# Optimization experiments

Measured on AMD Instinct MI355X. Metric: run time of the kernel, lower is better.

## Reference

```python
import jax, jax.numpy as jnp
import numpy as np

F = 128
NRBF = 20
CUTOFF = 5.0
L = 3
NZ = 100
F2 = F // 2
N = 10000
E = 256000
NMOL = 100
EPS = 1e-8


def setup_inputs() -> dict:
    key = jax.random.key(0)
    ks = jax.random.split(key, 20)
    xyz = jax.random.uniform(ks[0], (N, 3), jnp.float32) * 10.0
    z = jax.random.randint(ks[1], (N,), 0, NZ)
    nbrs = jax.random.randint(ks[2], (E, 2), 0, N)
    # avoid self-edges (would give zero distance in the sinc RBF)
    nbrs = nbrs.at[:, 1].set(jnp.where(nbrs[:, 1] == nbrs[:, 0], (nbrs[:, 1] + 1) % N, nbrs[:, 1]))
    mol_idx = jnp.sort(jax.random.randint(ks[3], (N,), 0, NMOL))

    def p(k, shape, scale=0.05):
        return jax.random.normal(k, shape, jnp.float32) * scale

    return dict(
        xyz=xyz, z=z, nbrs=nbrs, mol_idx=mol_idx,
        emb=p(ks[4], (NZ, F), 1.0),
        msg_W1=p(ks[5], (L, F, F)), msg_b1=jnp.zeros((L, F), jnp.float32),
        msg_W2=p(ks[6], (L, F, 3 * F)), msg_b2=jnp.zeros((L, 3 * F), jnp.float32),
        dist_W=p(ks[7], (L, NRBF, 3 * F)), dist_b=jnp.zeros((L, 3 * F), jnp.float32),
        upd_U=p(ks[8], (L, F, F)), upd_V=p(ks[9], (L, F, F)),
        upd_W1=p(ks[10], (L, 2 * F, F)), upd_b1=jnp.zeros((L, F), jnp.float32),
        upd_W2=p(ks[11], (L, F, 3 * F)), upd_b2=jnp.zeros((L, 3 * F), jnp.float32),
        read_W1=p(ks[12], (F, F2)), read_b1=jnp.zeros((F2,), jnp.float32),
        read_W2=p(ks[13], (F2, 1)), read_b2=jnp.zeros((1,), jnp.float32),
    )


def _painn(xyz, emb, msg_W1, msg_b1, msg_W2, msg_b2, dist_W, dist_b,
           upd_U, upd_V, upd_W1, upd_b1, upd_W2, upd_b2,
           read_W1, read_b1, read_W2, read_b2, z, nbrs, mol_idx):
    idx_i = nbrs[:, 0]
    idx_j = nbrs[:, 1]
    r_ij = xyz[idx_j] - xyz[idx_i]                       # [E,3]
    d = jnp.sqrt(jnp.sum(r_ij * r_ij, -1) + EPS)          # [E]
    unit = r_ij / d[:, None]
    # sinc radial basis + cosine cutoff envelope
    nvec = jnp.arange(1, NRBF + 1, dtype=xyz.dtype)
    rbf = jnp.sin(nvec[None, :] * jnp.pi * d[:, None] / CUTOFF) / d[:, None]   # [E,NRBF]
    fcut = 0.5 * (jnp.cos(jnp.pi * d / CUTOFF) + 1.0) * (d < CUTOFF)           # [E]

    s_i = emb[z]                                          # [N,F]
    v_i = jnp.zeros((xyz.shape[0], F, 3), xyz.dtype)      # [N,F,3]

    for l in range(L):
        # message block: invariant filter on nodes, gather to edges
        phi = (jax.nn.silu(s_i @ msg_W1[l] + msg_b1[l]) @ msg_W2[l] + msg_b2[l])[idx_j]  # [E,3F]
        w_s = (rbf @ dist_W[l] + dist_b[l]) * fcut[:, None]                               # [E,3F]
        inv = (phi * w_s).reshape(-1, 3, F)
        ds_edge = inv[:, 0]                                                               # [E,F]
        dv_edge = inv[:, 1][:, :, None] * v_i[idx_j] + inv[:, 2][:, :, None] * unit[:, None, :]  # [E,F,3]
        s_i = s_i + jax.ops.segment_sum(ds_edge, idx_i, num_segments=s_i.shape[0])
        v_i = v_i + jax.ops.segment_sum(dv_edge, idx_i, num_segments=s_i.shape[0])

        # update block: channel-mixing of vectors + gated scalar/vector residuals
        u_v = jnp.einsum('nfv,fg->ngv', v_i, upd_U[l])
        v_v = jnp.einsum('nfv,fg->ngv', v_i, upd_V[l])
        vnorm = jnp.sqrt(jnp.sum(v_v * v_v, -1) + EPS)                                    # [N,F]
        a = (jax.nn.silu(jnp.concatenate([s_i, vnorm], -1) @ upd_W1[l] + upd_b1[l])
             @ upd_W2[l] + upd_b2[l]).reshape(-1, 3, F)
        dv = u_v * a[:, 0][:, :, None]
        ds = a[:, 1] * jnp.sum(u_v * v_v, -1) + a[:, 2]
        s_i = s_i + ds
        v_i = v_i + dv

    atom_e = jax.nn.silu(s_i @ read_W1 + read_b1) @ read_W2 + read_b2                     # [N,1]
    energy = jax.ops.segment_sum(atom_e[:, 0], mol_idx, num_segments=NMOL)                # [NMOL]
    return energy


def reference(xyz, z, nbrs, mol_idx, emb, msg_W1, msg_b1, msg_W2, msg_b2,
              dist_W, dist_b, upd_U, upd_V, upd_W1, upd_b1, upd_W2, upd_b2,
              read_W1, read_b1, read_W2, read_b2):
    return _painn(xyz, emb, msg_W1, msg_b1, msg_W2, msg_b2, dist_W, dist_b,
                  upd_U, upd_V, upd_W1, upd_b1, upd_W2, upd_b2,
                  read_W1, read_b1, read_W2, read_b2, z, nbrs, mol_idx)
```

## Files before the change

kernel.cpp:

```cpp
#include <hip/hip_runtime.h>
#include <hip/hip_bf16.h>
#include <math.h>

#define NA 10000
#define NE 256000
#define FDIM 128
#define F3 384
#define NRBF 20
#define NLAYERS 3
#define NMOLS 100
#define CAP 96
#define WROW 388
#define PACK_BLOCKS 2288
#define CUTOFF_F 5.0f
#define EPS_F 1e-8f
#define PI_F 3.14159265358979323846f

typedef __attribute__((ext_vector_type(8))) short bf16x8;
typedef __attribute__((ext_vector_type(4))) float f32x4;

struct pv6 { unsigned int u0, u1, u2; };

__device__ __forceinline__ float silu_f(float x) { return x / (1.0f + __expf(-x)); }

__device__ __forceinline__ unsigned short f2bf(float x) {
  unsigned u = __float_as_uint(x);
  return (unsigned short)((u + 0x7FFFu + ((u >> 16) & 1u)) >> 16);
}
__device__ __forceinline__ float bf2f(unsigned short u) {
  return __uint_as_float(((unsigned)u) << 16);
}
__device__ __forceinline__ float lo_f(unsigned int u) { return bf2f((unsigned short)(u & 0xFFFFu)); }
__device__ __forceinline__ float hi_f(unsigned int u) { return bf2f((unsigned short)(u >> 16)); }

__device__ __forceinline__ void pack_one(const float* __restrict__ src,
                                         unsigned short* __restrict__ dst,
                                         int loc, int per, int N) {
  int lay = loc / per;
  int kn = loc - lay * per;
  int k = kn / N, n = kn - k * N;
  int kb = k >> 5, q = (k >> 3) & 3, j = k & 7, nt = n >> 4, c = n & 15;
  int NT = N >> 4;
  dst[(size_t)lay * per + (((kb * NT + nt) * 64 + (q * 16 + c)) * 8 + j)] = f2bf(src[loc]);
}

__device__ __forceinline__ void pack_dw(const float* __restrict__ dW,
                                        const float* __restrict__ db,
                                        unsigned short* __restrict__ dst, int loc) {
  int lay = loc / 12288;
  int kn = loc - lay * 12288;
  int k = kn / 384, n = kn - k * 384;
  float val = 0.0f;
  if (k < NRBF) val = dW[lay * NRBF * 384 + k * 384 + n];
  else if (k == NRBF) val = db[lay * 384 + n];
  int q = (k >> 3) & 3, j = k & 7, nt = n >> 4, c = n & 15;
  dst[(size_t)lay * 12288 + ((nt * 64 + (q * 16 + c)) * 8 + j)] = f2bf(val);
}

__global__ __launch_bounds__(256) void prep_kernel(
    const float* __restrict__ msgW1, const float* __restrict__ msgW2,
    const float* __restrict__ updU, const float* __restrict__ updV,
    const float* __restrict__ updW1, const float* __restrict__ updW2,
    const float* __restrict__ rW1, const float* __restrict__ distW,
    const float* __restrict__ distb, unsigned short* __restrict__ dst,
    const float* __restrict__ xyz, const int* __restrict__ nbrs,
    float* __restrict__ unitv, unsigned short* __restrict__ rbf_bf,
    float* __restrict__ fcut,
    int* __restrict__ deg, int* __restrict__ slot_e, int* __restrict__ slot_j) {
  int b = blockIdx.x;
  if (b < PACK_BLOCKS) {
    int t = b * 256 + threadIdx.x;
    if (t < 49152) pack_one(msgW1, dst, t, 16384, 128);
    else if (t < 196608) pack_one(msgW2, dst + 49152, t - 49152, 49152, 384);
    else if (t < 245760) pack_one(updU, dst + 196608, t - 196608, 16384, 128);
    else if (t < 294912) pack_one(updV, dst + 245760, t - 245760, 16384, 128);
    else if (t < 393216) pack_one(updW1, dst + 294912, t - 294912, 32768, 128);
    else if (t < 540672) pack_one(updW2, dst + 393216, t - 393216, 49152, 384);
    else if (t < 548864) pack_one(rW1, dst + 540672, t - 540672, 8192, 64);
    else if (t < 585728) pack_dw(distW, distb, dst + 548864, t - 548864);
    return;
  }
  int e = (b - PACK_BLOCKS) * 256 + threadIdx.x;
  if (e >= NE) return;
  int i = nbrs[2 * e + 0], j = nbrs[2 * e + 1];
  float rx = xyz[3 * j + 0] - xyz[3 * i + 0];
  float ry = xyz[3 * j + 1] - xyz[3 * i + 1];
  float rz = xyz[3 * j + 2] - xyz[3 * i + 2];
  float d = sqrtf(rx * rx + ry * ry + rz * rz + EPS_F);
  if (d >= CUTOFF_F) return;
  float invd = 1.0f / d;
  float fc = 0.5f * (__cosf(PI_F * d / CUTOFF_F) + 1.0f);
  unitv[3 * e + 0] = rx * invd;
  unitv[3 * e + 1] = ry * invd;
  unitv[3 * e + 2] = rz * invd;
  fcut[e] = fc;
  float base = PI_F * d / CUTOFF_F;
  float sc = invd * fc;
#pragma unroll
  for (int k = 0; k < NRBF; k++)
    rbf_bf[(size_t)e * NRBF + k] = f2bf(__sinf((float)(k + 1) * base) * sc);
  int pos = atomicAdd(&deg[i], 1);
  if (pos < CAP) {
    slot_e[i * CAP + pos] = e;
    slot_j[i * CAP + pos] = j;
  }
}

__global__ __launch_bounds__(256) void msg0_mfma_kernel(
    const float* __restrict__ emb, const int* __restrict__ z, float* __restrict__ s_out,
    const unsigned short* __restrict__ pW1, const float* __restrict__ b1,
    const unsigned short* __restrict__ pW2, const float* __restrict__ b2,
    pv6* __restrict__ cmb) {
  __shared__ bf16x8 sA[4 * 64];
  __shared__ bf16x8 hA[4 * 64];
  int a0 = blockIdx.x * 16;
  int t = threadIdx.x;
  int lane = t & 63, w = t >> 6;
  {
    int kb = t >> 6, l = t & 63;
    int m = l & 15, q = l >> 4;
    int zi = z[a0 + m];
    const float* sp = emb + (size_t)zi * FDIM + kb * 32 + q * 8;
    float* so = s_out + (size_t)(a0 + m) * FDIM + kb * 32 + q * 8;
    bf16x8 c;
#pragma unroll
    for (int j = 0; j < 8; j++) {
      float v = sp[j];
      so[j] = v;
      c[j] = (short)f2bf(v);
    }
    sA[kb * 64 + l] = c;
  }
  __syncthreads();
  f32x4 accH[2];
#pragma unroll
  for (int t2 = 0; t2 < 2; t2++)
#pragma unroll
    for (int r = 0; r < 4; r++) accH[t2][r] = 0.0f;
  const bf16x8* W1f = (const bf16x8*)pW1;
#pragma unroll
  for (int kb = 0; kb < 4; kb++) {
    bf16x8 a = sA[kb * 64 + lane];
#pragma unroll
    for (int t2 = 0; t2 < 2; t2++) {
      bf16x8 b = W1f[(kb * 8 + 2 * w + t2) * 64 + lane];
      accH[t2] = __builtin_amdgcn_mfma_f32_16x16x32_bf16(a, b, accH[t2], 0, 0, 0);
    }
  }
  short* hs = (short*)hA;
#pragma unroll
  for (int t2 = 0; t2 < 2; t2++) {
    int n = w * 32 + t2 * 16 + (lane & 15);
    int kb = n >> 5, q = (n >> 3) & 3, j = n & 7;
    float bias = b1[n];
#pragma unroll
    for (int r = 0; r < 4; r++) {
      int m = (lane >> 4) * 4 + r;
      hs[(kb * 64 + q * 16 + m) * 8 + j] = (short)f2bf(silu_f(accH[t2][r] + bias));
    }
  }
  __syncthreads();
  f32x4 accP[3][2];
#pragma unroll
  for (int c3 = 0; c3 < 3; c3++)
#pragma unroll
    for (int t2 = 0; t2 < 2; t2++)
#pragma unroll
      for (int r = 0; r < 4; r++) accP[c3][t2][r] = 0.0f;
  const bf16x8* W2f = (const bf16x8*)pW2;
#pragma unroll
  for (int kb = 0; kb < 4; kb++) {
    bf16x8 a = hA[kb * 64 + lane];
#pragma unroll
    for (int c3 = 0; c3 < 3; c3++)
#pragma unroll
      for (int t2 = 0; t2 < 2; t2++) {
        bf16x8 b = W2f[(kb * 24 + c3 * 8 + 2 * w + t2) * 64 + lane];
        accP[c3][t2] = __builtin_amdgcn_mfma_f32_16x16x32_bf16(a, b, accP[c3][t2], 0, 0, 0);
      }
  }
#pragma unroll
  for (int t2 = 0; t2 < 2; t2++) {
    int g = (2 * w + t2) * 16 + (lane & 15);
    float bb0 = b2[g], bb1 = b2[FDIM + g], bb2 = b2[2 * FDIM + g];
#pragma unroll
    for (int r = 0; r < 4; r++) {
      int m = (lane >> 4) * 4 + r;
      unsigned p0 = f2bf(accP[0][t2][r] + bb0);
      unsigned p1 = f2bf(accP[1][t2][r] + bb1);
      unsigned p2 = f2bf(accP[2][t2][r] + bb2);
      pv6 rec;
      rec.u0 = p0 | (p1 << 16);
      rec.u1 = p2;
      rec.u2 = 0;
      cmb[(size_t)(a0 + m) * FDIM + g] = rec;
    }
  }
}

__global__ __launch_bounds__(128) void edge_kernel(
    const pv6* __restrict__ cmb, unsigned short* __restrict__ v_lin,
    float* __restrict__ s, const unsigned short* __restrict__ pDW,
    const int* __restrict__ deg, const int* __restrict__ slot_e,
    const int* __restrict__ slot_j, const unsigned short* __restrict__ rbf_bf,
    const float* __restrict__ fcut, const float* __restrict__ unitv) {
  __shared__ bf16x8 aLDS[64];
  __shared__ unsigned short w_lds[16][WROW];
  __shared__ float l_u[16][3];
  __shared__ int l_j[16];
  int i = blockIdx.x;
  int t = threadIdx.x;
  int f = t;
  int lane = t & 63, w = t >> 6;
  int cnt = deg[i];
  if (cnt > CAP) cnt = CAP;
  int base = i * CAP;
  float acc_s = 0.f, av0 = 0.f, av1 = 0.f, av2 = 0.f;
  const bf16x8* Bf = (const bf16x8*)pDW;
  for (int c0 = 0; c0 < cnt; c0 += 16) {
    int ccnt = cnt - c0;
    if (ccnt > 16) ccnt = 16;
    __syncthreads();
    if (t < 64) {
      int m = t & 15, q = t >> 4;
      bf16x8 a;
#pragma unroll
      for (int j = 0; j < 8; j++) a[j] = 0;
      int p = c0 + m;
      if (p < cnt) {
        int e = slot_e[base + p];
        const unsigned short* rb = rbf_bf + (size_t)e * NRBF;
#pragma unroll
        for (int j = 0; j < 8; j++) {
          int k = q * 8 + j;
          if (k < NRBF) a[j] = (short)rb[k];
          else if (k == NRBF) a[j] = (short)f2bf(fcut[e]);
        }
      }
      aLDS[t] = a;
    } else if (t < 80) {
      int idx = t - 64;
      int p = c0 + idx;
      if (p < cnt) {
        int e = slot_e[base + p];
        l_j[idx] = slot_j[base + p];
        l_u[idx][0] = unitv[3 * e + 0];
        l_u[idx][1] = unitv[3 * e + 1];
        l_u[idx][2] = unitv[3 * e + 2];
      }
    }
    __syncthreads();
    {
      bf16x8 a = aLDS[lane];
      int n0 = lane & 15, m0 = (lane >> 4) * 4;
#pragma unroll
      for (int tt = 0; tt < 12; tt++) {
        int nt = 12 * w + tt;
        f32x4 acc;
#pragma unroll
        for (int r = 0; r < 4; r++) acc[r] = 0.0f;
        acc = __builtin_amdgcn_mfma_f32_16x16x32_bf16(a, Bf[nt * 64 + lane], acc, 0, 0, 0);
        int n = nt * 16 + n0;
#pragma unroll
        for (int r = 0; r < 4; r++) w_lds[m0 + r][n] = f2bf(acc[r]);
      }
    }
    __syncthreads();
    int pp = 0;
    for (; pp + 4 <= ccnt; pp += 4) {
      pv6 R[4];
#pragma unroll
      for (int u = 0; u < 4; u++) R[u] = cmb[(size_t)l_j[pp + u] * FDIM + f];
#pragma unroll
      for (int u = 0; u < 4; u++) {
        float p0 = lo_f(R[u].u0), p1 = hi_f(R[u].u0), p2 = lo_f(R[u].u1);
        float v0 = hi_f(R[u].u1), v1 = lo_f(R[u].u2), v2 = hi_f(R[u].u2);
        float w0 = bf2f(w_lds[pp + u][f]), w1 = bf2f(w_lds[pp + u][FDIM + f]),
              w2 = bf2f(w_lds[pp + u][2 * FDIM + f]);
        acc_s += p0 * w0;
        float i1 = p1 * w1, i2 = p2 * w2;
        av0 += i1 * v0 + i2 * l_u[pp + u][0];
        av1 += i1 * v1 + i2 * l_u[pp + u][1];
        av2 += i1 * v2 + i2 * l_u[pp + u][2];
      }
    }
    for (; pp < ccnt; pp++) {
      pv6 R0 = cmb[(size_t)l_j[pp] * FDIM + f];
      float p0 = lo_f(R0.u0), p1 = hi_f(R0.u0), p2 = lo_f(R0.u1);
      float v0 = hi_f(R0.u1), v1 = lo_f(R0.u2), v2 = hi_f(R0.u2);
      float w0 = bf2f(w_lds[pp][f]), w1 = bf2f(w_lds[pp][FDIM + f]),
            w2 = bf2f(w_lds[pp][2 * FDIM + f]);
      acc_s += p0 * w0;
      float i1 = p1 * w1, i2 = p2 * w2;
      av0 += i1 * v0 + i2 * l_u[pp][0];
      av1 += i1 * v1 + i2 * l_u[pp][1];
      av2 += i1 * v2 + i2 * l_u[pp][2];
    }
  }
  {
    pv6 RI = cmb[(size_t)i * FDIM + f];
    av0 += hi_f(RI.u1);
    av1 += lo_f(RI.u2);
    av2 += hi_f(RI.u2);
  }
  unsigned short* vlo = v_lin + (size_t)i * F3;
  vlo[f] = f2bf(av0);
  vlo[FDIM + f] = f2bf(av1);
  vlo[2 * FDIM + f] = f2bf(av2);
  s[(size_t)i * FDIM + f] += acc_s;
}

__global__ __launch_bounds__(256) void upd_fused_kernel(
    float* __restrict__ s, const unsigned short* __restrict__ v_lin,
    pv6* __restrict__ cmb,
    const unsigned short* __restrict__ pU, const unsigned short* __restrict__ pV,
    const unsigned short* __restrict__ pW1, const float* __restrict__ b1,
    const unsigned short* __restrict__ pW2, const float* __restrict__ b2,
    int mode,
    const unsigned short* __restrict__ pMW1, const float* __restrict__ mb1,
    const unsigned short* __restrict__ pMW2, const float* __restrict__ mb2,
    const unsigned short* __restrict__ pRW1, const float* __restrict__ rb1,
    const float* __restrict__ rW2, const float* __restrict__ rb2,
    float* __restrict__ atom_e) {
  __shared__ bf16x8 vAf[3 * 4 * 64];
  __shared__ bf16x8 catA[8 * 64];
  __shared__ bf16x8 hA[4 * 64];
  __shared__ float red[4][16];
  int a0 = blockIdx.x * 16;
  int t = threadIdx.x;
  int lane = t & 63, w = t >> 6;
  {
    int l = t & 63, kb = (t >> 6) & 3;
    int m = l & 15, q = l >> 4;
#pragma unroll
    for (int rt = 0; rt < 3; rt++) {
      vAf[(rt * 4 + kb) * 64 + l] =
          *(const bf16x8*)(v_lin + (size_t)(a0 + m) * F3 + rt * FDIM + kb * 32 + q * 8);
    }
    const float* sp = s + (size_t)(a0 + m) * FDIM + kb * 32 + q * 8;
    bf16x8 c;
#pragma unroll
    for (int j = 0; j < 8; j++) c[j] = (short)f2bf(sp[j]);
    catA[kb * 64 + l] = c;
  }
  __syncthreads();
  f32x4 accU[3][2], accV[3][2];
#pragma unroll
  for (int rt = 0; rt < 3; rt++)
#pragma unroll
    for (int t2 = 0; t2 < 2; t2++)
#pragma unroll
      for (int r = 0; r < 4; r++) { accU[rt][t2][r] = 0.0f; accV[rt][t2][r] = 0.0f; }
  const bf16x8* Uf = (const bf16x8*)pU;
  const bf16x8* Vf = (const bf16x8*)pV;
#pragma unroll
  for (int kb = 0; kb < 4; kb++) {
    bf16x8 bu[2], bv[2];
#pragma unroll
    for (int t2 = 0; t2 < 2; t2++) {
      bu[t2] = Uf[(kb * 8 + 2 * w + t2) * 64 + lane];
      bv[t2] = Vf[(kb * 8 + 2 * w + t2) * 64 + lane];
    }
#pragma unroll
    for (int rt = 0; rt < 3; rt++) {
      bf16x8 a = vAf[(rt * 4 + kb) * 64 + lane];
#pragma unroll
      for (int t2 = 0; t2 < 2; t2++) {
        accU[rt][t2] = __builtin_amdgcn_mfma_f32_16x16x32_bf16(a, bu[t2], accU[rt][t2], 0, 0, 0);
        accV[rt][t2] = __builtin_amdgcn_mfma_f32_16x16x32_bf16(a, bv[t2], accV[rt][t2], 0, 0, 0);
      }
    }
  }
  short* cs = (short*)catA;
#pragma unroll
  for (int t2 = 0; t2 < 2; t2++) {
    int g = w * 32 + t2 * 16 + (lane & 15);
    int k = 128 + g;
    int kb = k >> 5, q = (k >> 3) & 3, j = k & 7;
#pragma unroll
    for (int r = 0; r < 4; r++) {
      int m = (lane >> 4) * 4 + r;
      float x0 = accV[0][t2][r], x1 = accV[1][t2][r], x2 = accV[2][t2][r];
      cs[(kb * 64 + q * 16 + m) * 8 + j] = (short)f2bf(sqrtf(x0 * x0 + x1 * x1 + x2 * x2 + EPS_F));
    }
  }
  __syncthreads();
  f32x4 accH[2];
#pragma unroll
  for (int t2 = 0; t2 < 2; t2++)
#pragma unroll
    for (int r = 0; r < 4; r++) accH[t2][r] = 0.0f;
  const bf16x8* W1f = (const bf16x8*)pW1;
#pragma unroll
  for (int kb = 0; kb < 8; kb++) {
    bf16x8 a = catA[kb * 64 + lane];
#pragma unroll
    for (int t2 = 0; t2 < 2; t2++) {
      bf16x8 b = W1f[(kb * 8 + 2 * w + t2) * 64 + lane];
      accH[t2] = __builtin_amdgcn_mfma_f32_16x16x32_bf16(a, b, accH[t2], 0, 0, 0);
    }
  }
  short* hs = (short*)hA;
#pragma unroll
  for (int t2 = 0; t2 < 2; t2++) {
    int n = w * 32 + t2 * 16 + (lane & 15);
    int kb = n >> 5, q = (n >> 3) & 3, j = n & 7;
    float bias = b1[n];
#pragma unroll
    for (int r = 0; r < 4; r++) {
      int m = (lane >> 4) * 4 + r;
      hs[(kb * 64 + q * 16 + m) * 8 + j] = (short)f2bf(silu_f(accH[t2][r] + bias));
    }
  }
  __syncthreads();
  f32x4 accA[3][2];
#pragma unroll
  for (int c3 = 0; c3 < 3; c3++)
#pragma unroll
    for (int t2 = 0; t2 < 2; t2++)
#pragma unroll
      for (int r = 0; r < 4; r++) accA[c3][t2][r] = 0.0f;
  const bf16x8* W2f = (const bf16x8*)pW2;
#pragma unroll
  for (int kb = 0; kb < 4; kb++) {
    bf16x8 a = hA[kb * 64 + lane];
#pragma unroll
    for (int c3 = 0; c3 < 3; c3++)
#pragma unroll
      for (int t2 = 0; t2 < 2; t2++) {
        bf16x8 b = W2f[(kb * 24 + c3 * 8 + 2 * w + t2) * 64 + lane];
        accA[c3][t2] = __builtin_amdgcn_mfma_f32_16x16x32_bf16(a, b, accA[c3][t2], 0, 0, 0);
      }
  }
  const short* vls = (const short*)vAf;
  unsigned short v0keep[2][4];
#pragma unroll
  for (int t2 = 0; t2 < 2; t2++) {
    int g = w * 32 + t2 * 16 + (lane & 15);
    float bb0 = b2[g], bb1 = b2[FDIM + g], bb2 = b2[2 * FDIM + g];
    int kb = g >> 5, q = (g >> 3) & 3, j = g & 7;
#pragma unroll
    for (int r = 0; r < 4; r++) {
      int m = (lane >> 4) * 4 + r;
      int n = a0 + m;
      float a0v = accA[0][t2][r] + bb0;
      float a1v = accA[1][t2][r] + bb1;
      float a2v = accA[2][t2][r] + bb2;
      float dot = accU[0][t2][r] * accV[0][t2][r] + accU[1][t2][r] * accV[1][t2][r] +
                  accU[2][t2][r] * accV[2][t2][r];
      float s_new = s[(size_t)n * FDIM + g] + a1v * dot + a2v;
      if (mode == 0) {
        s[(size_t)n * FDIM + g] = s_new;
        float nv[3];
#pragma unroll
        for (int c = 0; c < 3; c++) {
          float vold = bf2f((unsigned short)vls[(((c * 4 + kb) * 64) + (q * 16 + m)) * 8 + j]);
          nv[c] = vold + a0v * accU[c][t2][r];
        }
        v0keep[t2][r] = f2bf(nv[0]);
        cmb[(size_t)n * FDIM + g].u2 = (unsigned)f2bf(nv[1]) | ((unsigned)f2bf(nv[2]) << 16);
      }
      cs[(kb * 64 + q * 16 + m) * 8 + j] = (short)f2bf(s_new);
    }
  }
  __syncthreads();
  if (mode == 0) {
    f32x4 accH2[2];
#pragma unroll
    for (int t2 = 0; t2 < 2; t2++)
#pragma unroll
      for (int r = 0; r < 4; r++) accH2[t2][r] = 0.0f;
    const bf16x8* MW1f = (const bf16x8*)pMW1;
#pragma unroll
    for (int kb = 0; kb < 4; kb++) {
      bf16x8 a = catA[kb * 64 + lane];
#pragma unroll
      for (int t2 = 0; t2 < 2; t2++) {
        bf16x8 b = MW1f[(kb * 8 + 2 * w + t2) * 64 + lane];
        accH2[t2] = __builtin_amdgcn_mfma_f32_16x16x32_bf16(a, b, accH2[t2], 0, 0, 0);
      }
    }
#pragma unroll
    for (int t2 = 0; t2 < 2; t2++) {
      int n = w * 32 + t2 * 16 + (lane & 15);
      int kb = n >> 5, q = (n >> 3) & 3, j = n & 7;
      float bias = mb1[n];
#pragma unroll
      for (int r = 0; r < 4; r++) {
        int m = (lane >> 4) * 4 + r;
        hs[(kb * 64 + q * 16 + m) * 8 + j] = (short)f2bf(silu_f(accH2[t2][r] + bias));
      }
    }
    __syncthreads();
    f32x4 accP[3][2];
#pragma unroll
    for (int c3 = 0; c3 < 3; c3++)
#pragma unroll
      for (int t2 = 0; t2 < 2; t2++)
#pragma unroll
        for (int r = 0; r < 4; r++) accP[c3][t2][r] = 0.0f;
    const bf16x8* MW2f = (const bf16x8*)pMW2;
#pragma unroll
    for (int kb = 0; kb < 4; kb++) {
      bf16x8 a = hA[kb * 64 + lane];
#pragma unroll
      for (int c3 = 0; c3 < 3; c3++)
#pragma unroll
        for (int t2 = 0; t2 < 2; t2++) {
          bf16x8 b = MW2f[(kb * 24 + c3 * 8 + 2 * w + t2) * 64 + lane];
          accP[c3][t2] = __builtin_amdgcn_mfma_f32_16x16x32_bf16(a, b, accP[c3][t2], 0, 0, 0);
        }
    }
#pragma unroll
    for (int t2 = 0; t2 < 2; t2++) {
      int g = (2 * w + t2) * 16 + (lane & 15);
      float bb0 = mb2[g], bb1 = mb2[FDIM + g], bb2v = mb2[2 * FDIM + g];
#pragma unroll
      for (int r = 0; r < 4; r++) {
        int m = (lane >> 4) * 4 + r;
        unsigned p0 = f2bf(accP[0][t2][r] + bb0);
        unsigned p1 = f2bf(accP[1][t2][r] + bb1);
        unsigned p2 = f2bf(accP[2][t2][r] + bb2v);
        pv6* rec = &cmb[(size_t)(a0 + m) * FDIM + g];
        rec->u0 = p0 | (p1 << 16);
        rec->u1 = p2 | ((unsigned)v0keep[t2][r] << 16);
      }
    }
  } else {
    f32x4 acc;
#pragma unroll
    for (int r = 0; r < 4; r++) acc[r] = 0.0f;
    const bf16x8* RW1f = (const bf16x8*)pRW1;
#pragma unroll
    for (int kb = 0; kb < 4; kb++) {
      bf16x8 a = catA[kb * 64 + lane];
      bf16x8 b = RW1f[(kb * 4 + w) * 64 + lane];
      acc = __builtin_amdgcn_mfma_f32_16x16x32_bf16(a, b, acc, 0, 0, 0);
    }
    int col = w * 16 + (lane & 15);
    float bias = rb1[col], w2v = rW2[col];
    float val[4];
#pragma unroll
    for (int r = 0; r < 4; r++) val[r] = silu_f(acc[r] + bias) * w2v;
#pragma unroll
    for (int off = 1; off < 16; off <<= 1)
#pragma unroll
      for (int r = 0; r < 4; r++) val[r] += __shfl_xor(val[r], off, 64);
    if ((lane & 15) == 0) {
#pragma unroll
      for (int r = 0; r < 4; r++) red[w][(lane >> 4) * 4 + r] = val[r];
    }
    __syncthreads();
    if (t < 16) {
      atom_e[a0 + t] = red[0][t] + red[1][t] + red[2][t] + red[3][t] + rb2[0];
    }
  }
}

__global__ __launch_bounds__(256) void mol_reduce_kernel(
    const float* __restrict__ atom_e, const int* __restrict__ mol_idx,
    float* __restrict__ out) {
  __shared__ float molsum[NMOLS];
  int t = threadIdx.x;
  if (t < NMOLS) molsum[t] = 0.0f;
  __syncthreads();
  int n = blockIdx.x * 256 + t;
  if (n < NA) atomicAdd(&molsum[mol_idx[n]], atom_e[n]);
  __syncthreads();
  if (t < NMOLS && molsum[t] != 0.0f) atomicAdd(&out[t], molsum[t]);
}

extern "C" void kernel_launch(void* const* d_in, const int* in_sizes, int n_in,
                              void* d_out, int out_size, void* d_ws, size_t ws_size,
                              hipStream_t stream) {
  const float* xyz = (const float*)d_in[0];
  const int* z = (const int*)d_in[1];
  const int* nbrs = (const int*)d_in[2];
  const int* mol = (const int*)d_in[3];
  const float* emb = (const float*)d_in[4];
  const float* msgW1 = (const float*)d_in[5];
  const float* msgb1 = (const float*)d_in[6];
  const float* msgW2 = (const float*)d_in[7];
  const float* msgb2 = (const float*)d_in[8];
  const float* distW = (const float*)d_in[9];
  const float* distb = (const float*)d_in[10];
  const float* updU = (const float*)d_in[11];
  const float* updV = (const float*)d_in[12];
  const float* updW1 = (const float*)d_in[13];
  const float* updb1 = (const float*)d_in[14];
  const float* updW2 = (const float*)d_in[15];
  const float* updb2 = (const float*)d_in[16];
  const float* rW1 = (const float*)d_in[17];
  const float* rb1 = (const float*)d_in[18];
  const float* rW2 = (const float*)d_in[19];
  const float* rb2 = (const float*)d_in[20];

  float* ws = (float*)d_ws;
  float* s = ws;      ws += (size_t)NA * FDIM;
  float* fcut = ws;   ws += (size_t)NE;
  float* unitv = ws;  ws += (size_t)NE * 3;
  float* atom_e = ws; ws += (size_t)NA;
  int* deg = (int*)ws;
  int* slot_e = deg + NA;
  int* slot_j = slot_e + NA * CAP;
  unsigned short* pk = (unsigned short*)(((uintptr_t)(slot_j + NA * CAP) + 15) & ~(uintptr_t)15);
  unsigned short* pMsgW1 = pk;
  unsigned short* pMsgW2 = pMsgW1 + 49152;
  unsigned short* pUpdU  = pMsgW2 + 147456;
  unsigned short* pUpdV  = pUpdU + 49152;
  unsigned short* pUpdW1 = pUpdV + 49152;
  unsigned short* pUpdW2 = pUpdW1 + 98304;
  unsigned short* pRW1   = pUpdW2 + 147456;
  unsigned short* pDW    = pRW1 + 8192;
  unsigned short* rbf_bf = (unsigned short*)(((uintptr_t)(pDW + 36864) + 15) & ~(uintptr_t)15);
  unsigned short* after_rbf = rbf_bf + (size_t)NE * NRBF + 8;
  pv6* cmb = (pv6*)(((uintptr_t)after_rbf + 15) & ~(uintptr_t)15);
  unsigned short* v_lin = (unsigned short*)(cmb + (size_t)NA * FDIM);

  hipMemsetAsync(deg, 0, NA * sizeof(int), stream);
  hipMemsetAsync(d_out, 0, NMOLS * sizeof(float), stream);

  prep_kernel<<<PACK_BLOCKS + NE / 256, 256, 0, stream>>>(
      msgW1, msgW2, updU, updV, updW1, updW2, rW1, distW, distb, pMsgW1,
      xyz, nbrs, unitv, rbf_bf, fcut, deg, slot_e, slot_j);
  msg0_mfma_kernel<<<NA / 16, 256, 0, stream>>>(emb, z, s, pMsgW1, msgb1, pMsgW2, msgb2, cmb);

  for (int l = 0; l < NLAYERS; l++) {
    edge_kernel<<<NA, 128, 0, stream>>>(cmb, v_lin, s,
                                        pDW + (size_t)l * 12288,
                                        deg, slot_e, slot_j, rbf_bf, fcut, unitv);
    int mode = (l == NLAYERS - 1) ? 1 : 0;
    int lnext = (l + 1 < NLAYERS) ? l + 1 : 0;
    upd_fused_kernel<<<NA / 16, 256, 0, stream>>>(
        s, v_lin, cmb, pUpdU + (size_t)l * 16384, pUpdV + (size_t)l * 16384,
        pUpdW1 + (size_t)l * 32768, updb1 + (size_t)l * FDIM,
        pUpdW2 + (size_t)l * 49152, updb2 + (size_t)l * F3,
        mode,
        pMsgW1 + (size_t)lnext * 16384, msgb1 + (size_t)lnext * FDIM,
        pMsgW2 + (size_t)lnext * 49152, msgb2 + (size_t)lnext * F3,
        pRW1, rb1, rW2, rb2, atom_e);
  }
  mol_reduce_kernel<<<(NA + 255) / 256, 256, 0, stream>>>(atom_e, mol, (float*)d_out);
}
```

Measured before the change: 298.9 us.

## Use sine recurrence for RBF, restructure edge staging, fuse molecule reduction

The RBF computation now uses a Chebyshev-style recurrence from a single sincos instead of twenty separate sine evaluations. The edge kernel preloads all neighbour edge and j indices into LDS once per atom. Each wave also builds its own MFMA A fragment directly, which removes the aLDS staging array and one barrier per chunk. The separate molecule-reduction kernel is removed and per-atom energies are atomically added to the output inside the final update kernel; this saves a launch but trades it for more global atomics, and the recurrence may accumulate slightly more rounding error.

```diff
diff --git a/kernel.cpp b/kernel.cpp
--- a/kernel.cpp
+++ b/kernel.cpp
@@ -96,9 +96,20 @@
   fcut[e] = fc;
   float base = PI_F * d / CUTOFF_F;
   float sc = invd * fc;
-#pragma unroll
-  for (int k = 0; k < NRBF; k++)
-    rbf_bf[(size_t)e * NRBF + k] = f2bf(__sinf((float)(k + 1) * base) * sc);
+  {
+    float s1, c1;
+    __sincosf(base, &s1, &c1);
+    float twoc = 2.0f * c1;
+    float skm = 0.0f, sk = s1;
+    rbf_bf[(size_t)e * NRBF + 0] = f2bf(sk * sc);
+#pragma unroll
+    for (int k = 1; k < NRBF; k++) {
+      float sk1 = twoc * sk - skm;
+      skm = sk;
+      sk = sk1;
+      rbf_bf[(size_t)e * NRBF + k] = f2bf(sk * sc);
+    }
+  }
   int pos = atomicAdd(&deg[i], 1);
   if (pos < CAP) {
     slot_e[i * CAP + pos] = e;
@@ -204,10 +215,10 @@
     const int* __restrict__ deg, const int* __restrict__ slot_e,
     const int* __restrict__ slot_j, const unsigned short* __restrict__ rbf_bf,
     const float* __restrict__ fcut, const float* __restrict__ unitv) {
-  __shared__ bf16x8 aLDS[64];
-  __shared__ unsigned short w_lds[16][WROW];
+  __shared__ __align__(16) unsigned short w_lds[16][WROW];
   __shared__ float l_u[16][3];
-  __shared__ int l_j[16];
+  __shared__ int l_e_all[CAP];
+  __shared__ int l_j_all[CAP];
   int i = blockIdx.x;
   int t = threadIdx.x;
   int f = t;
@@ -215,44 +226,44 @@
   int cnt = deg[i];
   if (cnt > CAP) cnt = CAP;
   int base = i * CAP;
+  if (t < cnt) {
+    l_e_all[t] = slot_e[base + t];
+    l_j_all[t] = slot_j[base + t];
+  }
+  __syncthreads();
   float acc_s = 0.f, av0 = 0.f, av1 = 0.f, av2 = 0.f;
   const bf16x8* Bf = (const bf16x8*)pDW;
+  int m16 = lane & 15, q4 = lane >> 4;
   for (int c0 = 0; c0 < cnt; c0 += 16) {
     int ccnt = cnt - c0;
     if (ccnt > 16) ccnt = 16;
-    __syncthreads();
-    if (t < 64) {
-      int m = t & 15, q = t >> 4;
-      bf16x8 a;
-#pragma unroll
-      for (int j = 0; j < 8; j++) a[j] = 0;
-      int p = c0 + m;
+    if (c0) __syncthreads();
+    if (t >= 64 && t < 80) {
+      int idx = t - 64, p = c0 + idx;
       if (p < cnt) {
-        int e = slot_e[base + p];
-        const unsigned short* rb = rbf_bf + (size_t)e * NRBF;
-#pragma unroll
-        for (int j = 0; j < 8; j++) {
-          int k = q * 8 + j;
-          if (k < NRBF) a[j] = (short)rb[k];
-          else if (k == NRBF) a[j] = (short)f2bf(fcut[e]);
-        }
-      }
-      aLDS[t] = a;
-    } else if (t < 80) {
-      int idx = t - 64;
-      int p = c0 + idx;
-      if (p < cnt) {
-        int e = slot_e[base + p];
-        l_j[idx] = slot_j[base + p];
+        int e = l_e_all[p];
         l_u[idx][0] = unitv[3 * e + 0];
         l_u[idx][1] = unitv[3 * e + 1];
         l_u[idx][2] = unitv[3 * e + 2];
       }
     }
-    __syncthreads();
+    bf16x8 a;
+#pragma unroll
+    for (int j = 0; j < 8; j++) a[j] = 0;
+    if (q4 < 3 && m16 < ccnt) {
+      int e = l_e_all[c0 + m16];
+      const unsigned short* rb = rbf_bf + (size_t)e * NRBF;
+      if (q4 < 2) {
+#pragma unroll
+        for (int j = 0; j < 8; j++) a[j] = (short)rb[q4 * 8 + j];
+      } else {
+#pragma unroll
+        for (int j = 0; j < 4; j++) a[j] = (short)rb[16 + j];
+        a[4] = (short)f2bf(fcut[e]);
+      }
+    }
     {
-      bf16x8 a = aLDS[lane];
-      int n0 = lane & 15, m0 = (lane >> 4) * 4;
+      int mrow = q4 * 4;
 #pragma unroll
       for (int tt = 0; tt < 12; tt++) {
         int nt = 12 * w + tt;
@@ -260,9 +271,9 @@
 #pragma unroll
         for (int r = 0; r < 4; r++) acc[r] = 0.0f;
         acc = __builtin_amdgcn_mfma_f32_16x16x32_bf16(a, Bf[nt * 64 + lane], acc, 0, 0, 0);
-        int n = nt * 16 + n0;
-#pragma unroll
-        for (int r = 0; r < 4; r++) w_lds[m0 + r][n] = f2bf(acc[r]);
+        int n = nt * 16 + m16;
+#pragma unroll
+        for (int r = 0; r < 4; r++) w_lds[mrow + r][n] = f2bf(acc[r]);
       }
     }
     __syncthreads();
@@ -270,7 +281,7 @@
     for (; pp + 4 <= ccnt; pp += 4) {
       pv6 R[4];
 #pragma unroll
-      for (int u = 0; u < 4; u++) R[u] = cmb[(size_t)l_j[pp + u] * FDIM + f];
+      for (int u = 0; u < 4; u++) R[u] = cmb[(size_t)l_j_all[c0 + pp + u] * FDIM + f];
 #pragma unroll
       for (int u = 0; u < 4; u++) {
         float p0 = lo_f(R[u].u0), p1 = hi_f(R[u].u0), p2 = lo_f(R[u].u1);
@@ -285,7 +296,7 @@
       }
     }
     for (; pp < ccnt; pp++) {
-      pv6 R0 = cmb[(size_t)l_j[pp] * FDIM + f];
+      pv6 R0 = cmb[(size_t)l_j_all[c0 + pp] * FDIM + f];
       float p0 = lo_f(R0.u0), p1 = hi_f(R0.u0), p2 = lo_f(R0.u1);
       float v0 = hi_f(R0.u1), v1 = lo_f(R0.u2), v2 = hi_f(R0.u2);
       float w0 = bf2f(w_lds[pp][f]), w1 = bf2f(w_lds[pp][FDIM + f]),
@@ -321,7 +332,7 @@
     const unsigned short* __restrict__ pMW2, const float* __restrict__ mb2,
     const unsigned short* __restrict__ pRW1, const float* __restrict__ rb1,
     const float* __restrict__ rW2, const float* __restrict__ rb2,
-    float* __restrict__ atom_e) {
+    const int* __restrict__ mol_idx, float* __restrict__ out) {
   __shared__ bf16x8 vAf[3 * 4 * 64];
   __shared__ bf16x8 catA[8 * 64];
   __shared__ bf16x8 hA[4 * 64];
@@ -552,22 +563,10 @@
     }
     __syncthreads();
     if (t < 16) {
-      atom_e[a0 + t] = red[0][t] + red[1][t] + red[2][t] + red[3][t] + rb2[0];
-    }
-  }
-}
-
-__global__ __launch_bounds__(256) void mol_reduce_kernel(
-    const float* __restrict__ atom_e, const int* __restrict__ mol_idx,
-    float* __restrict__ out) {
-  __shared__ float molsum[NMOLS];
-  int t = threadIdx.x;
-  if (t < NMOLS) molsum[t] = 0.0f;
-  __syncthreads();
-  int n = blockIdx.x * 256 + t;
-  if (n < NA) atomicAdd(&molsum[mol_idx[n]], atom_e[n]);
-  __syncthreads();
-  if (t < NMOLS && molsum[t] != 0.0f) atomicAdd(&out[t], molsum[t]);
+      float ae = red[0][t] + red[1][t] + red[2][t] + red[3][t] + rb2[0];
+      atomicAdd(&out[mol_idx[a0 + t]], ae);
+    }
+  }
 }
 
 extern "C" void kernel_launch(void* const* d_in, const int* in_sizes, int n_in,
@@ -599,7 +598,6 @@
   float* s = ws;      ws += (size_t)NA * FDIM;
   float* fcut = ws;   ws += (size_t)NE;
   float* unitv = ws;  ws += (size_t)NE * 3;
-  float* atom_e = ws; ws += (size_t)NA;
   int* deg = (int*)ws;
   int* slot_e = deg + NA;
   int* slot_j = slot_e + NA * CAP;
@@ -638,7 +636,6 @@
         mode,
         pMsgW1 + (size_t)lnext * 16384, msgb1 + (size_t)lnext * FDIM,
         pMsgW2 + (size_t)lnext * 49152, msgb2 + (size_t)lnext * F3,
-        pRW1, rb1, rW2, rb2, atom_e);
-  }
-  mol_reduce_kernel<<<(NA + 255) / 256, 256, 0, stream>>>(atom_e, mol, (float*)d_out);
-}
+        pRW1, rb1, rW2, rb2, mol, (float*)d_out);
+  }
+}
```

After: 331.4 us. 1.11x slower.
